# Performance work log

Measured on AMD Instinct MI355X. Metric: run time of the kernel, lower is better.

## Reference

```python
import jax, jax.numpy as jnp
import numpy as np

B, T, C, H = 1024, 256, 384, 64  # batch, block_size, n_embd, head_size


def _rope_tables():
    # standard rotary tables: theta_i = 10000^(-2i/H), angles = pos * theta
    inv_freq = 1.0 / (10000.0 ** (jnp.arange(0, H, 2, dtype=jnp.float32) / H))  # [H/2]
    pos = jnp.arange(T, dtype=jnp.float32)
    ang = pos[:, None] * inv_freq[None, :]          # [T, H/2]
    ang = jnp.concatenate([ang, ang], axis=-1)       # [T, H]
    return jnp.cos(ang), jnp.sin(ang)


def setup_inputs() -> dict:
    key = jax.random.key(0)
    kx, kq, kk, kv = jax.random.split(key, 4)
    cos, sin = _rope_tables()
    s = 1.0 / np.sqrt(C)
    return {
        "x": jax.random.normal(kx, (B, T, C), dtype=jnp.float32),
        "cos": cos,
        "sin": sin,
        "Wq": jax.random.normal(kq, (C, H), dtype=jnp.float32) * s,
        "Wk": jax.random.normal(kk, (C, H), dtype=jnp.float32) * s,
        "Wv": jax.random.normal(kv, (C, H), dtype=jnp.float32) * s,
    }


def _rotary(x, cos, sin):
    # x: [B, T, H]; cos/sin: [T, H]
    half = x.shape[-1] // 2
    x1, x2 = x[..., :half], x[..., half:]
    rotated = jnp.concatenate([-x2, x1], axis=-1)
    return x * cos + rotated * sin


def reference(x, cos, sin, Wq, Wk, Wv):
    Tn = x.shape[1]
    q = x @ Wq                                  # [B,T,H]
    k = x @ Wk
    v = x @ Wv
    q = _rotary(q, cos[:Tn], sin[:Tn])
    k = _rotary(k, cos[:Tn], sin[:Tn])
    scale = k.shape[-1] ** -0.5
    wei = jnp.einsum('btd,bsd->bts', q, k) * scale  # [B,T,T] — materialized as in original
    causal = jnp.tril(jnp.ones((Tn, Tn), dtype=bool))
    wei = jnp.where(causal, wei, -jnp.inf)
    wei = jax.nn.softmax(wei, axis=-1)
    # dropout omitted (eval mode / deterministic reference)
    out = jnp.einsum('bts,bsd->btd', wei, v)    # [B,T,H]
    return out
```

## Files before the change

kernel.cpp:

```cpp
#include <hip/hip_runtime.h>
#include <hip/hip_bf16.h>


typedef __attribute__((ext_vector_type(8))) short bf16x8;
typedef __attribute__((ext_vector_type(4))) float f32x4;

#define B_ 1024
#define T_ 256
#define C_ 384
#define H_ 64

static __device__ __forceinline__ unsigned short f2bf(float f) {
  unsigned int u = __float_as_uint(f);
  return (unsigned short)((u + 0x7fffu + ((u >> 16) & 1u)) >> 16);
}

static __device__ __forceinline__ float bf2f(unsigned short h) {
  return __uint_as_float(((unsigned int)h) << 16);
}

static __device__ __forceinline__ bf16x8 cvt8(float4 a, float4 b) {
  union { __hip_bfloat162 h[4]; bf16x8 v; } u;
  u.h[0] = __float22bfloat162_rn(make_float2(a.x, a.y));
  u.h[1] = __float22bfloat162_rn(make_float2(a.z, a.w));
  u.h[2] = __float22bfloat162_rn(make_float2(b.x, b.y));
  u.h[3] = __float22bfloat162_rn(make_float2(b.z, b.w));
  return u.v;
}

__global__ void pack_w_frag(const float* __restrict__ Wq, const float* __restrict__ Wk,
                            const float* __restrict__ Wv, unsigned short* __restrict__ wtp) {
  int id = blockIdx.x * 256 + threadIdx.x;
  if (id >= 144 * 512) return;
  int i = id & 7, lane = (id >> 3) & 63, f = id >> 9;
  int nt = f % 12, ks = f / 12;
  int n = nt * 16 + (lane & 15);
  int k = ks * 32 + (lane >> 4) * 8 + i;
  const float* W = (n < 64) ? Wq : ((n < 128) ? Wk : Wv);
  wtp[id] = f2bf(W[k * 64 + (n & 63)]);
}

__launch_bounds__(512, 6)
__global__ void qkv_kernel(const float* __restrict__ x, const float* __restrict__ cosp,
                           const float* __restrict__ sinp,
                           const unsigned short* __restrict__ wtp,
                           unsigned short* __restrict__ qp,
                           unsigned short* __restrict__ kp,
                           unsigned short* __restrict__ vp) {
  __shared__ __align__(16) unsigned short xs[64 * 384];

  unsigned short* Qst = xs;
  unsigned short* Kst = xs + 64 * 72;
  unsigned short* Vst = xs + 2 * 64 * 72;

  const int tid = threadIdx.x;
  const int w = tid >> 6;
  const int lane = tid & 63;
  const int l15 = lane & 15;
  const int lq = lane >> 4;
  const int bk = blockIdx.x;
  const int b = bk >> 2, g64 = bk & 3;
  const int row0 = g64 * 64;

  const float* xb = x + (size_t)b * T_ * C_ + (size_t)row0 * C_;

  {
    float4 c0[2], c1[2];
    {
      const float* p = xb + (size_t)tid * 8;
      c0[0] = *(const float4*)p;
      c0[1] = *(const float4*)(p + 4);
    }
    #pragma unroll
    for (int s = 0; s < 6; ++s) {
      if (s + 1 < 6) {
        const float* p = xb + (size_t)((s + 1) * 512 + tid) * 8;
        c1[0] = *(const float4*)p;
        c1[1] = *(const float4*)(p + 4);
      }
      int c = s * 512 + tid;
      int row = c / 48;
      int cb = (c - row * 48) * 16;
      bf16x8 v = cvt8(c0[0], c0[1]);
      *(bf16x8*)((char*)xs + row * 768 + (cb ^ ((row & 7) << 4))) = v;
      c0[0] = c1[0]; c0[1] = c1[1];
    }
  }
  __syncthreads();

  const int ng = w & 3, rset = w >> 2;

  f32x4 acc[2][3];
  #pragma unroll
  for (int i = 0; i < 2; ++i)
    #pragma unroll
    for (int m = 0; m < 3; ++m) {
      f32x4 z = {0.f, 0.f, 0.f, 0.f};
      acc[i][m] = z;
    }

  const int arow0 = (rset * 2) * 16 + l15;
  const int arow1 = (rset * 2 + 1) * 16 + l15;
  const char* xrow0 = (const char*)xs + arow0 * 768;
  const char* xrow1 = (const char*)xs + arow1 * 768;
  const int asw0 = (arow0 & 7) << 4;
  const int asw1 = (arow1 & 7) << 4;

  #pragma unroll
  for (int ks = 0; ks < 12; ++ks) {
    bf16x8 bv[3];
    #pragma unroll
    for (int m = 0; m < 3; ++m)
      bv[m] = *(const bf16x8*)(wtp + ((size_t)(ks * 12 + ng * 3 + m) * 64 + lane) * 8);
    bf16x8 a0 = *(const bf16x8*)(xrow0 + ((ks * 64 + lq * 16) ^ asw0));
    bf16x8 a1 = *(const bf16x8*)(xrow1 + ((ks * 64 + lq * 16) ^ asw1));
    #pragma unroll
    for (int m = 0; m < 3; ++m) {
      acc[0][m] = __builtin_amdgcn_mfma_f32_16x16x32_bf16(a0, bv[m], acc[0][m], 0, 0, 0);
      acc[1][m] = __builtin_amdgcn_mfma_f32_16x16x32_bf16(a1, bv[m], acc[1][m], 0, 0, 0);
    }
  }
  __syncthreads();

  #pragma unroll
  for (int i = 0; i < 2; ++i) {
    #pragma unroll
    for (int m = 0; m < 3; ++m) {
      const int nt = ng * 3 + m;
      #pragma unroll
      for (int j = 0; j < 4; ++j) {
        const int r64 = (rset * 2 + i) * 16 + lq * 4 + j;
        unsigned short v = f2bf(acc[i][m][j]);
        if (nt < 4)      Qst[r64 * 72 + nt * 16 + l15] = v;
        else if (nt < 8) Kst[r64 * 72 + (nt - 4) * 16 + l15] = v;
        else             Vst[((nt - 8) * 16 + l15) * 72 + r64] = v;
      }
    }
  }
  __syncthreads();

  #pragma unroll
  for (int pass = 0; pass < 3; ++pass) {
    const int id = pass * 8 + w;
    if (id < 16) {
      const unsigned short* S = (id < 8) ? Qst : Kst;
      unsigned short* dst = (id < 8) ? qp : kp;
      const int lid = id & 7;
      const int tl = lid >> 1;
      const int ks2 = lid & 1;
      const int r64 = tl * 16 + l15;
      const int c0 = ks2 * 32 + lq * 8;
      const unsigned short* rowp = S + r64 * 72;
      bf16x8 mv = *(const bf16x8*)(rowp + c0);
      bf16x8 pv = *(const bf16x8*)(rowp + (c0 ^ 32));
      const int tglob = row0 + r64;
      const float* cp = cosp + tglob * H_ + c0;
      const float* sp = sinp + tglob * H_ + c0;
      float4 ca = *(const float4*)cp, cb = *(const float4*)(cp + 4);
      float4 sa = *(const float4*)sp, sb = *(const float4*)(sp + 4);
      const float sgn = ks2 ? 1.0f : -1.0f;
      bf16x8 ov;
      ov[0] = (short)f2bf(bf2f((unsigned short)mv[0]) * ca.x + sgn * bf2f((unsigned short)pv[0]) * sa.x);
      ov[1] = (short)f2bf(bf2f((unsigned short)mv[1]) * ca.y + sgn * bf2f((unsigned short)pv[1]) * sa.y);
      ov[2] = (short)f2bf(bf2f((unsigned short)mv[2]) * ca.z + sgn * bf2f((unsigned short)pv[2]) * sa.z);
      ov[3] = (short)f2bf(bf2f((unsigned short)mv[3]) * ca.w + sgn * bf2f((unsigned short)pv[3]) * sa.w);
      ov[4] = (short)f2bf(bf2f((unsigned short)mv[4]) * cb.x + sgn * bf2f((unsigned short)pv[4]) * sb.x);
      ov[5] = (short)f2bf(bf2f((unsigned short)mv[5]) * cb.y + sgn * bf2f((unsigned short)pv[5]) * sb.y);
      ov[6] = (short)f2bf(bf2f((unsigned short)mv[6]) * cb.z + sgn * bf2f((unsigned short)pv[6]) * sb.z);
      ov[7] = (short)f2bf(bf2f((unsigned short)mv[7]) * cb.w + sgn * bf2f((unsigned short)pv[7]) * sb.w);
      const int tile_glob = g64 * 4 + tl;
      *(bf16x8*)(dst + ((((size_t)b * 16 + tile_glob) * 2 + ks2) * 64 + lane) * 8) = ov;
    } else if (id < 24) {
      const int lid = id - 16;
      const int ntv = lid >> 1;
      const int kgl = lid & 1;
      const int ksg = g64 * 2 + kgl;
      bf16x8 fr = *(const bf16x8*)(Vst + (ntv * 16 + l15) * 72 + kgl * 32 + lq * 8);
      *(bf16x8*)(vp + ((((size_t)b * 4 + ntv) * 8 + ksg) * 64 + lane) * 8) = fr;
    }
  }
}

__launch_bounds__(256, 4)
__global__ void attn_kernel(const unsigned short* __restrict__ qp,
                            const unsigned short* __restrict__ kp,
                            const unsigned short* __restrict__ vp,
                            float* __restrict__ out) {
  __shared__ unsigned short Plds[4 * 16 * 264];

  const int tid = threadIdx.x;
  const int w = tid >> 6;
  const int lane = tid & 63;
  const int l15 = lane & 15;
  const int lq = lane >> 4;
  const int bk = blockIdx.x;
  const int b = bk >> 1, half = bk & 1;
  const int rt2[2] = {half * 8 + w, half * 8 + 7 - w};

  unsigned short* Pw = Plds + w * 16 * 264;
  float* ob = out + (size_t)b * T_ * H_;

  #pragma unroll
  for (int i = 0; i < 2; ++i) {
    const int ti = rt2[i];
    const int t0 = ti * 16;

    bf16x8 aq[2];
    #pragma unroll
    for (int ks2 = 0; ks2 < 2; ++ks2)
      aq[ks2] = *(const bf16x8*)(qp + ((((size_t)b * 16 + ti) * 2 + ks2) * 64 + lane) * 8);

    f32x4 sacc[16];
    #pragma unroll
    for (int si = 0; si < 16; ++si) {
      f32x4 z = {0.f, 0.f, 0.f, 0.f};
      sacc[si] = z;
    }

    #pragma unroll
    for (int si = 0; si < 16; ++si) {
      if (si <= ti) {
        #pragma unroll
        for (int ks2 = 0; ks2 < 2; ++ks2) {
          bf16x8 bkf = *(const bf16x8*)(kp + ((((size_t)b * 16 + si) * 2 + ks2) * 64 + lane) * 8);
          sacc[si] = __builtin_amdgcn_mfma_f32_16x16x32_bf16(aq[ks2], bkf, sacc[si], 0, 0, 0);
        }
      }
    }

    int trow = t0 + lq * 4;
    #pragma unroll
    for (int si = 0; si < 16; ++si) {
      #pragma unroll
      for (int j = 0; j < 4; ++j) {
        float s = sacc[si][j] * 0.125f;
        if (si * 16 + l15 > trow + j) s = -1e30f;
        sacc[si][j] = s;
      }
    }

    float rl[4];
    #pragma unroll
    for (int j = 0; j < 4; ++j) {
      float mj = -1e30f;
      #pragma unroll
      for (int si = 0; si < 16; ++si) mj = fmaxf(mj, sacc[si][j]);
      #pragma unroll
      for (int d = 1; d < 16; d <<= 1) mj = fmaxf(mj, __shfl_xor(mj, d));
      float lj = 0.0f;
      #pragma unroll
      for (int si = 0; si < 16; ++si) {
        float p = __expf(sacc[si][j] - mj);
        lj += p;
        Pw[(lq * 4 + j) * 264 + si * 16 + l15] = f2bf(p);
      }
      #pragma unroll
      for (int d = 1; d < 16; d <<= 1) lj += __shfl_xor(lj, d);
      rl[j] = 1.0f / lj;
    }

    f32x4 oacc[4];
    #pragma unroll
    for (int nt = 0; nt < 4; ++nt) {
      f32x4 z = {0.f, 0.f, 0.f, 0.f};
      oacc[nt] = z;
    }
    int nk = (t0 + 16 + 31) >> 5;
    for (int ks = 0; ks < nk; ++ks) {
      bf16x8 ap = *(const bf16x8*)&Pw[l15 * 264 + ks * 32 + lq * 8];
      #pragma unroll
      for (int nt = 0; nt < 4; ++nt) {
        bf16x8 bv = *(const bf16x8*)(vp + ((((size_t)b * 4 + nt) * 8 + ks) * 64 + lane) * 8);
        oacc[nt] = __builtin_amdgcn_mfma_f32_16x16x32_bf16(ap, bv, oacc[nt], 0, 0, 0);
      }
    }

    #pragma unroll
    for (int nt = 0; nt < 4; ++nt)
      #pragma unroll
      for (int j = 0; j < 4; ++j)
        ob[(t0 + lq * 4 + j) * H_ + nt * 16 + l15] = oacc[nt][j] * rl[j];
  }
}

extern "C" void kernel_launch(void* const* d_in, const int* in_sizes, int n_in,
                              void* d_out, int out_size, void* d_ws, size_t ws_size,
                              hipStream_t stream) {
  const float* x    = (const float*)d_in[0];
  const float* cosp = (const float*)d_in[1];
  const float* sinp = (const float*)d_in[2];
  const float* Wq   = (const float*)d_in[3];
  const float* Wk   = (const float*)d_in[4];
  const float* Wv   = (const float*)d_in[5];
  float* out = (float*)d_out;

  const size_t wtp_bytes = 144 * 512 * 2;
  const size_t frag_elems = (size_t)B_ * 16 * 2 * 64 * 8;

  unsigned short* wtp = (unsigned short*)d_ws;
  unsigned short* qp = (unsigned short*)((char*)d_ws + wtp_bytes);
  unsigned short* kp = qp + frag_elems;
  unsigned short* vp = kp + frag_elems;
  (void)ws_size;

  pack_w_frag<<<288, 256, 0, stream>>>(Wq, Wk, Wv, wtp);
  qkv_kernel<<<4096, 512, 0, stream>>>(x, cosp, sinp, wtp, qp, kp, vp);
  attn_kernel<<<B_ * 2, 256, 0, stream>>>(qp, kp, vp, out);
}
```

Before: 205.1 us.

## Split x tile load into halves to overlap second-half loads with MFMA

Loads the first half of the columns of the x tile into LDS, issues global loads for the second half into registers, and runs the first six k-steps of the QKV projection MFMA while those loads are in flight. It then converts and stores the second half and runs the remaining k-steps. The aim is to hide global memory latency behind compute. In exchange it holds 24 more float registers per thread, which can reduce occupancy, and adds a second block barrier.

```diff
diff --git a/kernel.cpp b/kernel.cpp
--- a/kernel.cpp
+++ b/kernel.cpp
@@ -64,32 +64,41 @@
 
   const float* xb = x + (size_t)b * T_ * C_ + (size_t)row0 * C_;
 
+  auto addrH = [&](int c, int h) -> const float* {
+    int row = c / 24, col = c - row * 24 + h * 24;
+    return xb + (size_t)row * C_ + col * 8;
+  };
+  auto ldsH = [&](int c, int h) -> char* {
+    int row = c / 24, col = c - row * 24 + h * 24;
+    return (char*)xs + row * 768 + ((col * 16) ^ ((row & 7) << 4));
+  };
+
   {
-    float4 c0[2], c1[2];
+    float4 ca[2], cn[2];
     {
-      const float* p = xb + (size_t)tid * 8;
-      c0[0] = *(const float4*)p;
-      c0[1] = *(const float4*)(p + 4);
-    }
-    #pragma unroll
-    for (int s = 0; s < 6; ++s) {
-      if (s + 1 < 6) {
-        const float* p = xb + (size_t)((s + 1) * 512 + tid) * 8;
-        c1[0] = *(const float4*)p;
-        c1[1] = *(const float4*)(p + 4);
-      }
-      int c = s * 512 + tid;
-      int row = c / 48;
-      int cb = (c - row * 48) * 16;
-      bf16x8 v = cvt8(c0[0], c0[1]);
-      *(bf16x8*)((char*)xs + row * 768 + (cb ^ ((row & 7) << 4))) = v;
-      c0[0] = c1[0]; c0[1] = c1[1];
-    }
+      const float* p = addrH(tid, 0);
+      ca[0] = *(const float4*)p; ca[1] = *(const float4*)(p + 4);
+    }
+    #pragma unroll
+    for (int s = 0; s < 3; ++s) {
+      if (s + 1 < 3) {
+        const float* p = addrH((s + 1) * 512 + tid, 0);
+        cn[0] = *(const float4*)p; cn[1] = *(const float4*)(p + 4);
+      }
+      *(bf16x8*)ldsH(s * 512 + tid, 0) = cvt8(ca[0], ca[1]);
+      ca[0] = cn[0]; ca[1] = cn[1];
+    }
+  }
+
+  float4 pb[3][2];
+  #pragma unroll
+  for (int s = 0; s < 3; ++s) {
+    const float* p = addrH(s * 512 + tid, 1);
+    pb[s][0] = *(const float4*)p; pb[s][1] = *(const float4*)(p + 4);
   }
   __syncthreads();
 
   const int ng = w & 3, rset = w >> 2;
-
   f32x4 acc[2][3];
   #pragma unroll
   for (int i = 0; i < 2; ++i)
@@ -107,7 +116,27 @@
   const int asw1 = (arow1 & 7) << 4;
 
   #pragma unroll
-  for (int ks = 0; ks < 12; ++ks) {
+  for (int ks = 0; ks < 6; ++ks) {
+    bf16x8 bv[3];
+    #pragma unroll
+    for (int m = 0; m < 3; ++m)
+      bv[m] = *(const bf16x8*)(wtp + ((size_t)(ks * 12 + ng * 3 + m) * 64 + lane) * 8);
+    bf16x8 a0 = *(const bf16x8*)(xrow0 + ((ks * 64 + lq * 16) ^ asw0));
+    bf16x8 a1 = *(const bf16x8*)(xrow1 + ((ks * 64 + lq * 16) ^ asw1));
+    #pragma unroll
+    for (int m = 0; m < 3; ++m) {
+      acc[0][m] = __builtin_amdgcn_mfma_f32_16x16x32_bf16(a0, bv[m], acc[0][m], 0, 0, 0);
+      acc[1][m] = __builtin_amdgcn_mfma_f32_16x16x32_bf16(a1, bv[m], acc[1][m], 0, 0, 0);
+    }
+  }
+
+  #pragma unroll
+  for (int s = 0; s < 3; ++s)
+    *(bf16x8*)ldsH(s * 512 + tid, 1) = cvt8(pb[s][0], pb[s][1]);
+  __syncthreads();
+
+  #pragma unroll
+  for (int ks = 6; ks < 12; ++ks) {
     bf16x8 bv[3];
     #pragma unroll
     for (int m = 0; m < 3; ++m)
```

Result: slower. 241.5 us (+17.8%).
